# Kernel tuning notes

Hardware: AMD Instinct MI355X
Metric: run time of the kernel (lower is better)

Reference implementation:

```python
import jax, jax.numpy as jnp
import numpy as np

N, D, DOUT = 10000, 128, 128
KS, KN, KC, NCENTER, HID = 32, 16, 16, 3, 32  # HID = D // 4


def setup_inputs() -> dict:
    key = jax.random.key(0)
    ks = jax.random.split(key, 32)
    p = lambda i, shape: jax.random.normal(ks[i], shape, dtype=jnp.float32) * 0.05
    return {
        "ids": jnp.arange(N, dtype=jnp.int64) if jax.config.jax_enable_x64 else jnp.arange(N, dtype=jnp.int32),
        "feats": jax.random.normal(ks[0], (N, D), dtype=jnp.float32),
        "cluster_idx": jax.random.randint(ks[1], (N, NCENTER, KC), 0, N),
        "struct_idx": jax.random.randint(ks[2], (N, KS), 0, N),
        "epo": 100,
        # VertexConv (cluster): Transform convKK grouped conv -> (k,k,D) weight, (k,k) bias; convK1 -> (k,) weight, scalar bias
        "wKK_c": p(3, (KC, KC, D)), "bKK_c": p(4, (KC, KC)), "wK1_c": p(5, (KC,)), "bK1_c": p(6, ()),
        # VertexConv (knn)
        "wKK_n": p(7, (KN, KN, D)), "bKK_n": p(8, (KN, KN)), "wK1_n": p(9, (KN,)), "bK1_n": p(10, ()),
        # VertexConv (structure)
        "wKK_s": p(11, (KS, KS, D)), "bKK_s": p(12, (KS, KS)), "wK1_s": p(13, (KS,)), "bK1_s": p(14, ()),
        # EdgeConv attention MLP: Linear(D, D//4) -> ReLU -> Linear(D//4, 1)
        "ec_w1": p(15, (D, HID)), "ec_b1": p(16, (HID,)), "ec_w2": p(17, (HID,)), "ec_b2": p(18, ()),
        # Final Linear(D, DOUT)
        "fc_w": p(19, (D, DOUT)), "fc_b": p(20, (DOUT,)),
    }


def vertex_conv(x, wKK, bKK, wK1, bK1):
    # x: (N, k, d). Grouped Conv1d(k, k*k, d, groups=k): mult[n,i,j] = <wKK[i,j], x[n,i]> + bKK[i,j]
    mult = jnp.einsum("nid,ijd->nij", x, wKK) + bKK
    mult = jax.nn.softmax(mult, axis=-1)                 # softmax over last dim
    transformed = jnp.einsum("nij,njd->nid", mult, x)    # (N, k, d)
    # Conv1d(k, 1, 1): weighted sum over the k channels
    return jnp.einsum("nkd,k->nd", transformed, wK1) + bK1


def reference(ids, feats, cluster_idx, struct_idx, epo,
              wKK_c, bKK_c, wK1_c, bK1_c,
              wKK_n, bKK_n, wK1_n, bK1_n,
              wKK_s, bKK_s, wK1_s, bK1_s,
              ec_w1, ec_b1, ec_w2, ec_b2, fc_w, fc_b):
    # epo=100 >= all warmups -> all three hyperedge branches active (static).
    # --- cluster hyperedges (precomputed kmeans index table) ---
    c_feats = feats[cluster_idx[ids]]                    # (N, n_center, kc, d)
    hyperedge = [vertex_conv(c_feats[:, c], wKK_c, bKK_c, wK1_c, bK1_c)
                 for c in range(NCENTER)]
    # --- knn hyperedge: cosine similarity + topk (cos_dis) ---
    nrm = jnp.maximum(jnp.linalg.norm(feats, axis=1, keepdims=True), 1e-12)
    xn = feats / nrm
    sim = xn @ xn.T                                      # (N, N) -- memory-dominant
    _, knn_idx = jax.lax.top_k(sim, KN)                  # (N, kn)
    hyperedge.append(vertex_conv(feats[knn_idx[ids]], wKK_n, bKK_n, wK1_n, bK1_n))
    # --- structure hyperedge (precomputed sampled edge_dict table) ---
    hyperedge.append(vertex_conv(feats[struct_idx[ids]], wKK_s, bKK_s, wK1_s, bK1_s))
    x = jnp.stack(hyperedge, axis=1)                     # (N, t, d), t = n_center + 2
    # EdgeConv: MLP attention over the t hyperedges, softmax along t, weighted sum
    h = jax.nn.relu(jnp.einsum("ntd,dh->nth", x, ec_w1) + ec_b1)
    scores = jax.nn.softmax(jnp.einsum("nth,h->nt", h, ec_w2) + ec_b2, axis=1)
    agg = jnp.einsum("nt,ntd->nd", scores, x)            # (N, d)
    # final fc + relu (dropout = identity in eval)
    return jax.nn.relu(agg @ fc_w + fc_b)
```

## Files before the change

kernel.cpp:

```cpp
#include <hip/hip_runtime.h>
#include <cmath>


#define N_NODES 10000
#define D 128
#define DQ 32
#define NCB 3
#define T_HE 5
#define HID_SZ 32
#define NCH 16
#define CHUNK 625
#define TILE 64
#define TPC 10
#define TOPK 16
#define TOPM 32

typedef __attribute__((ext_vector_type(8))) short short8;
typedef __attribute__((ext_vector_type(8))) _Float16 half8;
typedef __attribute__((ext_vector_type(4))) float f32x4;
typedef __attribute__((ext_vector_type(16))) float f32x16;

__device__ __forceinline__ unsigned bf16rne(float f) {
  unsigned u = __float_as_uint(f);
  return (u + 0x7FFFu + ((u >> 16) & 1u)) >> 16;
}

__global__ __launch_bounds__(256) void kpre(const float* __restrict__ feats,
                                            const float* __restrict__ wc,
                                            const float* __restrict__ wn,
                                            const float* __restrict__ wstr,
                                            unsigned short* __restrict__ xnh,
                                            _Float16* __restrict__ fH16,
                                            double* __restrict__ normD,
                                            _Float16* __restrict__ wH16) {
  int bx = blockIdx.x;
  int tid = threadIdx.x;
  if (bx < 2500) {
    int n = bx * 4 + (tid >> 6);
    int lane = tid & 63;
    float2 v = ((const float2*)(feats + (size_t)n * D))[lane];
    _Float16 p2[2] = {(_Float16)v.x, (_Float16)v.y};
    ((unsigned*)(fH16 + (size_t)n * D))[lane] = *(const unsigned*)p2;
    double ss = (double)v.x * (double)v.x + (double)v.y * (double)v.y;
#pragma unroll
    for (int o = 32; o > 0; o >>= 1) ss += __shfl_xor(ss, o);
    double nd = fmax(sqrt(ss), 1e-12);
    if (lane == 0) normD[n] = nd;
    float inv = (float)(1.0 / nd);
    ((unsigned*)(xnh + (size_t)n * D))[lane] = bf16rne(v.x * inv) | (bf16rne(v.y * inv) << 16);
  } else {
    int p = (bx - 2500) * 256 + tid;
    if (p >= 98304) return;
    int e = p * 2;
    float2 v;
    if (e < 32768) v = *(const float2*)(wc + e);
    else if (e < 65536) v = *(const float2*)(wn + (e - 32768));
    else v = *(const float2*)(wstr + (e - 65536));
    _Float16 p2[2] = {(_Float16)v.x, (_Float16)v.y};
    ((unsigned*)wH16)[p] = *(const unsigned*)p2;
  }
}

__device__ __forceinline__ void ceu(unsigned& a, unsigned& b) {
  unsigned lo = min(a, b), hi = max(a, b);
  a = lo; b = hi;
}
__device__ __forceinline__ void ceu64(unsigned long long& a, unsigned long long& b) {
  unsigned long long lo = min(a, b), hi = max(a, b);
  a = lo; b = hi;
}
__device__ __forceinline__ void oems16_asc(unsigned (&v)[16]) {
  ceu(v[0], v[1]); ceu(v[2], v[3]); ceu(v[0], v[2]); ceu(v[1], v[3]); ceu(v[1], v[2]);
  ceu(v[4], v[5]); ceu(v[6], v[7]); ceu(v[4], v[6]); ceu(v[5], v[7]); ceu(v[5], v[6]);
  ceu(v[0], v[4]); ceu(v[2], v[6]); ceu(v[2], v[4]); ceu(v[1], v[5]); ceu(v[3], v[7]);
  ceu(v[3], v[5]); ceu(v[1], v[2]); ceu(v[3], v[4]); ceu(v[5], v[6]);
  ceu(v[8], v[9]); ceu(v[10], v[11]); ceu(v[8], v[10]); ceu(v[9], v[11]); ceu(v[9], v[10]);
  ceu(v[12], v[13]); ceu(v[14], v[15]); ceu(v[12], v[14]); ceu(v[13], v[15]); ceu(v[13], v[14]);
  ceu(v[8], v[12]); ceu(v[10], v[14]); ceu(v[10], v[12]); ceu(v[9], v[13]); ceu(v[11], v[15]);
  ceu(v[11], v[13]); ceu(v[9], v[10]); ceu(v[11], v[12]); ceu(v[13], v[14]);
  ceu(v[0], v[8]); ceu(v[4], v[12]); ceu(v[4], v[8]); ceu(v[2], v[10]); ceu(v[6], v[14]);
  ceu(v[6], v[10]); ceu(v[2], v[4]); ceu(v[6], v[8]); ceu(v[10], v[12]);
  ceu(v[1], v[9]); ceu(v[5], v[13]); ceu(v[5], v[9]); ceu(v[3], v[11]); ceu(v[7], v[15]);
  ceu(v[7], v[11]); ceu(v[3], v[5]); ceu(v[7], v[9]); ceu(v[11], v[13]);
  ceu(v[1], v[2]); ceu(v[3], v[4]); ceu(v[5], v[6]); ceu(v[7], v[8]); ceu(v[9], v[10]);
  ceu(v[11], v[12]); ceu(v[13], v[14]);
}
__device__ __forceinline__ void merge16_asc(unsigned (&run)[16], const unsigned (&b)[16]) {
  unsigned m[16];
#pragma unroll
  for (int i = 0; i < 16; i++) m[i] = max(run[i], b[15 - i]);
#pragma unroll
  for (int j = 8; j > 0; j >>= 1) {
#pragma unroll
    for (int i = 0; i < 16; i++) {
      if ((i & j) == 0) ceu(m[i], m[i + j]);
    }
  }
#pragma unroll
  for (int i = 0; i < 16; i++) run[i] = m[i];
}

__device__ __forceinline__ void vc16_body(int tid, int n0, int tslot,
    int* idxLm, float* coefPm, float* coefSm,
    const _Float16* __restrict__ fH16, const _Float16* __restrict__ wH16,
    const int* __restrict__ idxTab, int istr, int ioff, int woff,
    const float* __restrict__ bKK, const float* __restrict__ wK1,
    const float* __restrict__ bK1p, float* __restrict__ hx) {
  int w = tid >> 6, lane = tid & 63, l15 = lane & 15, quad = lane >> 4;
  const half8* fH = (const half8*)fH16;
  {
    int nn = tid >> 4, i = tid & 15;
    idxLm[nn * 33 + i] = idxTab[(size_t)(n0 + nn) * istr + ioff + i];
  }
  __syncthreads();
  const half8* wHv = (const half8*)(wH16 + woff);
  f32x4 coef = {0.f, 0.f, 0.f, 0.f};
#pragma unroll
  for (int ii = 0; ii < 4; ii++) {
    int i = w * 4 + ii;
    int rowi = idxLm[l15 * 33 + i];
    float bkk = bKK[i * 16 + l15];
    f32x4 acc = {0.f, 0.f, 0.f, 0.f};
#pragma unroll
    for (int kc = 0; kc < 4; kc++) {
      half8 ah = fH[(size_t)rowi * 16 + kc * 4 + quad];
      half8 bh = wHv[((size_t)i * 16 + l15) * 16 + kc * 4 + quad];
      acc = __builtin_amdgcn_mfma_f32_16x16x32_f16(ah, bh, acc, 0, 0, 0);
    }
    float wki = wK1[i];
#pragma unroll
    for (int r = 0; r < 4; r++) {
      float v = acc[r] + bkk;
      float mx = v;
#pragma unroll
      for (int msk = 1; msk < 16; msk <<= 1) mx = fmaxf(mx, __shfl_xor(mx, msk));
      float e = __expf(v - mx);
      float s = e;
#pragma unroll
      for (int msk = 1; msk < 16; msk <<= 1) s += __shfl_xor(s, msk);
      coef[r] += wki * (e / s);
    }
  }
#pragma unroll
  for (int r = 0; r < 4; r++) coefPm[(w * 16 + quad * 4 + r) * 33 + l15] = coef[r];
  __syncthreads();
  {
    int nn = tid >> 4, j = tid & 15;
    coefSm[nn * 33 + j] = coefPm[(nn) * 33 + j] + coefPm[(16 + nn) * 33 + j] +
                          coefPm[(32 + nn) * 33 + j] + coefPm[(48 + nn) * 33 + j];
  }
  __syncthreads();
  {
    int nl = tid >> 4, g = tid & 15;
    float bk1 = bK1p[0];
    float a8[8];
#pragma unroll
    for (int t = 0; t < 8; t++) a8[t] = bk1;
    for (int j = 0; j < 16; j++) {
      float cf = coefSm[nl * 33 + j];
      int rowj = idxLm[nl * 33 + j];
      half8 xv = fH[(size_t)rowj * 16 + g];
#pragma unroll
      for (int e = 0; e < 8; e++) a8[e] = fmaf(cf, (float)xv[e], a8[e]);
    }
    int node = n0 + nl;
    float4* o = (float4*)(hx + ((size_t)node * T_HE + tslot) * D + g * 8);
    o[0] = make_float4(a8[0], a8[1], a8[2], a8[3]);
    o[1] = make_float4(a8[4], a8[5], a8[6], a8[7]);
  }
}

__device__ __forceinline__ void vc32_body(int tid, int n0,
    int* idxLm, float* coefPm, float* coefSm,
    const _Float16* __restrict__ fH16, const _Float16* __restrict__ wH16,
    const int* __restrict__ struct_idx,
    const float* __restrict__ bKK_s, const float* __restrict__ wK1_s,
    const float* __restrict__ bK1_s, float* __restrict__ hx) {
  int w = tid >> 6, lane = tid & 63, l15 = lane & 15, quad = lane >> 4;
  const half8* fH = (const half8*)fH16;
  for (int e = tid; e < 512; e += 256) {
    int nn = e >> 5, i = e & 31;
    idxLm[nn * 33 + i] = struct_idx[(size_t)(n0 + nn) * 32 + i];
  }
  __syncthreads();
  const half8* wHv = (const half8*)(wH16 + 65536);
  f32x4 coef0 = {0.f, 0.f, 0.f, 0.f};
  f32x4 coef1 = {0.f, 0.f, 0.f, 0.f};
#pragma unroll
  for (int ii = 0; ii < 8; ii++) {
    int i = w * 8 + ii;
    int rowi = idxLm[l15 * 33 + i];
    float bk0 = bKK_s[i * 32 + l15];
    float bk1v = bKK_s[i * 32 + 16 + l15];
    f32x4 a0 = {0.f, 0.f, 0.f, 0.f};
    f32x4 a1 = {0.f, 0.f, 0.f, 0.f};
#pragma unroll
    for (int kc = 0; kc < 4; kc++) {
      half8 ah = fH[(size_t)rowi * 16 + kc * 4 + quad];
      half8 b0 = wHv[((size_t)i * 32 + l15) * 16 + kc * 4 + quad];
      half8 b1 = wHv[((size_t)i * 32 + 16 + l15) * 16 + kc * 4 + quad];
      a0 = __builtin_amdgcn_mfma_f32_16x16x32_f16(ah, b0, a0, 0, 0, 0);
      a1 = __builtin_amdgcn_mfma_f32_16x16x32_f16(ah, b1, a1, 0, 0, 0);
    }
    float wki = wK1_s[i];
#pragma unroll
    for (int r = 0; r < 4; r++) {
      float v0 = a0[r] + bk0, v1 = a1[r] + bk1v;
      float mx = fmaxf(v0, v1);
#pragma unroll
      for (int msk = 1; msk < 16; msk <<= 1) mx = fmaxf(mx, __shfl_xor(mx, msk));
      float e0 = __expf(v0 - mx), e1 = __expf(v1 - mx);
      float s = e0 + e1;
#pragma unroll
      for (int msk = 1; msk < 16; msk <<= 1) s += __shfl_xor(s, msk);
      float inv = wki / s;
      coef0[r] += e0 * inv;
      coef1[r] += e1 * inv;
    }
  }
#pragma unroll
  for (int r = 0; r < 4; r++) {
    coefPm[(w * 16 + quad * 4 + r) * 33 + l15] = coef0[r];
    coefPm[(w * 16 + quad * 4 + r) * 33 + l15 + 16] = coef1[r];
  }
  __syncthreads();
  for (int e = tid; e < 512; e += 256) {
    int nn = e >> 5, j = e & 31;
    coefSm[nn * 33 + j] = coefPm[nn * 33 + j] + coefPm[(16 + nn) * 33 + j] +
                          coefPm[(32 + nn) * 33 + j] + coefPm[(48 + nn) * 33 + j];
  }
  __syncthreads();
  {
    int nl = tid >> 4, g = tid & 15;
    float bk1 = bK1_s[0];
    float a8[8];
#pragma unroll
    for (int t = 0; t < 8; t++) a8[t] = bk1;
    for (int j = 0; j < 32; j++) {
      float cf = coefSm[nl * 33 + j];
      int rowj = idxLm[nl * 33 + j];
      half8 xv = fH[(size_t)rowj * 16 + g];
#pragma unroll
      for (int e = 0; e < 8; e++) a8[e] = fmaf(cf, (float)xv[e], a8[e]);
    }
    int node = n0 + nl;
    float4* o = (float4*)(hx + ((size_t)node * T_HE + 4) * D + g * 8);
    o[0] = make_float4(a8[0], a8[1], a8[2], a8[3]);
    o[1] = make_float4(a8[4], a8[5], a8[6], a8[7]);
  }
}

__global__ __launch_bounds__(256, 3) void ksimvc(
    const unsigned short* __restrict__ xnh, unsigned* __restrict__ cand,
    const _Float16* __restrict__ fH16, const _Float16* __restrict__ wH16,
    const int* __restrict__ cluster_idx, const int* __restrict__ struct_idx,
    const float* __restrict__ bKK_c, const float* __restrict__ bKK_s,
    const float* __restrict__ wK1_c, const float* __restrict__ bK1_c,
    const float* __restrict__ wK1_s, const float* __restrict__ bK1_s,
    float* __restrict__ hx) {
  __shared__ __align__(16) unsigned char smem[16384];
  int bx = blockIdx.x;
  int tid = threadIdx.x;
  int r3 = bx % 3, q3 = bx / 3;
  if (r3 == 0) {
    int sid = q3;
    int rb = sid % 79, chunk = sid / 79;
    int w = tid >> 6, lane = tid & 63, l31 = lane & 31, lh = lane >> 5;
    int row0 = rb * 128 + w * 32;
    int cbase = chunk * CHUNK;
    int ci = tid >> 2, q = tid & 3;
    short8* bp = (short8*)smem;
    const short8* bv = (const short8*)smem;

    short8 afr[8];
    {
      int ar = min(row0 + l31, N_NODES - 1);
      const short8* ap = (const short8*)(xnh + (size_t)ar * D);
#pragma unroll
      for (int ks = 0; ks < 8; ks++) afr[ks] = ap[ks * 2 + lh];
    }

    unsigned run[16];
#pragma unroll
    for (int s = 0; s < 16; s++) run[s] = 0u;

    short8 G[4];
    {
      int gcol = min(cbase + ci, N_NODES - 1);
      const short8* gp = (const short8*)(xnh + (size_t)gcol * D);
#pragma unroll
      for (int i = 0; i < 4; i++) G[i] = gp[q * 4 + i];
    }

#pragma unroll 1
    for (int ti = 0; ti < TPC; ti++) {
      __syncthreads();
      {
#pragma unroll
        for (int i = 0; i < 4; i++) bp[(q * 4 + i) * 64 + ci] = G[i];
      }
      if (ti + 1 < TPC) {
        int gcol = min(cbase + (ti + 1) * TILE + ci, N_NODES - 1);
        const short8* gp = (const short8*)(xnh + (size_t)gcol * D);
#pragma unroll
        for (int i = 0; i < 4; i++) G[i] = gp[q * 4 + i];
      }
      __syncthreads();

#pragma unroll
      for (int ni = 0; ni < 2; ni++) {
        f32x16 acc;
#pragma unroll
        for (int r = 0; r < 16; r++) acc[r] = 2.0f;
#pragma unroll
        for (int ks = 0; ks < 8; ks++) {
          short8 af = bv[(ks * 2 + lh) * 64 + ni * 32 + l31];
          acc = __builtin_amdgcn_mfma_f32_32x32x16_bf16(af, afr[ks], acc, 0, 0, 0);
        }
        unsigned bt[16];
#pragma unroll
        for (int reg = 0; reg < 16; reg++) {
          int m = (reg & 3) + 8 * (reg >> 2) + 4 * lh;
          unsigned bb = __float_as_uint(acc[reg]);
          bt[reg] = (bb & 0xFFFFFC00u) | (unsigned)(ti * TILE + ni * 32 + m);
        }
        if (ti == TPC - 1) {
#pragma unroll
          for (int reg = 0; reg < 16; reg++) {
            int m = (reg & 3) + 8 * (reg >> 2) + 4 * lh;
            if (ni * 32 + m >= CHUNK - (TPC - 1) * TILE) bt[reg] = 0u;
          }
        }
        oems16_asc(bt);
        merge16_asc(run, bt);
      }
    }
    {
      unsigned other[16];
#pragma unroll
      for (int s = 0; s < 16; s++) other[s] = (unsigned)__shfl_xor((int)run[s], 32);
      merge16_asc(run, other);
    }
    int grow = row0 + l31;
    if (lh == 0 && grow < N_NODES) {
      unsigned* o = cand + ((size_t)chunk * N_NODES + grow) * 16;
#pragma unroll
      for (int i = 0; i < 16; i += 4)
        *(uint4*)(o + i) = make_uint4(run[i], run[i + 1], run[i + 2], run[i + 3]);
    }
  } else {
    int vid = q3 * 2 + (r3 - 1);
    if (vid >= 2500) return;
    int zz = vid / 625, bi = vid - zz * 625;
    int n0 = bi * 16;
    int* idxLm = (int*)smem;
    float* coefPm = (float*)(smem + 2112);
    float* coefSm = (float*)(smem + 10560);
    if (zz < 3) {
      vc16_body(tid, n0, zz, idxLm, coefPm, coefSm, fH16, wH16,
                cluster_idx, NCB * 16, zz * 16, 0, bKK_c, wK1_c, bK1_c, hx);
    } else {
      vc32_body(tid, n0, idxLm, coefPm, coefSm, fH16, wH16,
                struct_idx, bKK_s, wK1_s, bK1_s, hx);
    }
  }
}

__global__ __launch_bounds__(256, 4) void kvc3(
    const _Float16* __restrict__ fH16, const _Float16* __restrict__ wH16,
    const int* __restrict__ knn,
    const float* __restrict__ bKK_n, const float* __restrict__ wK1_n,
    const float* __restrict__ bK1_n, float* __restrict__ hx) {
  __shared__ __align__(16) unsigned char smem[12672];
  int* idxLm = (int*)smem;
  float* coefPm = (float*)(smem + 2112);
  float* coefSm = (float*)(smem + 10560);
  vc16_body(threadIdx.x, blockIdx.x * 16, 3, idxLm, coefPm, coefSm, fH16, wH16,
            knn, 16, 0, 32768, bKK_n, wK1_n, bK1_n, hx);
}

__global__ __launch_bounds__(256) void kmerge(const unsigned* __restrict__ cand,
                                              int* __restrict__ candIdx) {
  int t4 = blockIdx.x * 256 + threadIdx.x;
  int row = t4 >> 2, sub = t4 & 3;
  if (row >= N_NODES) return;
  unsigned long long run[TOPM];
#pragma unroll
  for (int s = 0; s < TOPM; s++) run[s] = 0ull;
  const uint4* c4 = (const uint4*)cand;
#pragma unroll
  for (int t = 0; t < 4; t++) {
    int ch = sub * 4 + t;
    unsigned b[16];
#pragma unroll
    for (int q = 0; q < 4; q++) {
      uint4 v = c4[((size_t)ch * N_NODES + row) * 4 + q];
      b[q * 4 + 0] = v.x; b[q * 4 + 1] = v.y;
      b[q * 4 + 2] = v.z; b[q * 4 + 3] = v.w;
    }
    unsigned base = (unsigned)(ch * CHUNK);
    unsigned long long b64[16];
#pragma unroll
    for (int s = 0; s < 16; s++) {
      unsigned k = b[s];
      b64[s] = ((unsigned long long)(k >> 10) << 32) |
               (unsigned long long)(base + (k & 1023u));
    }
#pragma unroll
    for (int i = 0; i < 16; i++) run[i] = max(run[i], b64[15 - i]);
#pragma unroll
    for (int j = 16; j > 0; j >>= 1)
#pragma unroll
      for (int i = 0; i < TOPM; i++)
        if ((i & j) == 0) ceu64(run[i], run[i + j]);
  }
#pragma unroll
  for (int off = 1; off <= 2; off <<= 1) {
    unsigned long long oth[TOPM];
#pragma unroll
    for (int s = 0; s < TOPM; s++) {
      unsigned lo = (unsigned)(run[s] & 0xFFFFFFFFull);
      unsigned hi = (unsigned)(run[s] >> 32);
      lo = (unsigned)__shfl_xor((int)lo, off);
      hi = (unsigned)__shfl_xor((int)hi, off);
      oth[s] = ((unsigned long long)hi << 32) | (unsigned long long)lo;
    }
#pragma unroll
    for (int i = 0; i < TOPM; i++) run[i] = max(run[i], oth[TOPM - 1 - i]);
#pragma unroll
    for (int j = 16; j > 0; j >>= 1)
#pragma unroll
      for (int i = 0; i < TOPM; i++)
        if ((i & j) == 0) ceu64(run[i], run[i + j]);
  }
  if (sub == 0) {
    int4* o4 = (int4*)(candIdx + (size_t)row * TOPM);
#pragma unroll
    for (int s = 0; s < TOPM; s += 4) {
      int4 o;
      o.x = (int)(unsigned)(run[s + 0] & 0xFFFFFFFFull);
      o.y = (int)(unsigned)(run[s + 1] & 0xFFFFFFFFull);
      o.z = (int)(unsigned)(run[s + 2] & 0xFFFFFFFFull);
      o.w = (int)(unsigned)(run[s + 3] & 0xFFFFFFFFull);
      o4[s >> 2] = o;
    }
  }
}

__global__ __launch_bounds__(256) void krerank(const float* __restrict__ feats,
                                               const double* __restrict__ normD,
                                               const int* __restrict__ candIdx,
                                               int* __restrict__ knn) {
  __shared__ float rowF[D];
  __shared__ double simL[TOPM];
  __shared__ int idxL[TOPM];
  int row = blockIdx.x;
  int tid = threadIdx.x;
  if (tid < DQ)
    ((float4*)rowF)[tid] = ((const float4*)(feats + (size_t)row * D))[tid];
  int c = tid >> 3, part = tid & 7;
  int cnd = candIdx[(size_t)row * TOPM + c];
  __syncthreads();
  const float4* f4 = (const float4*)(feats + (size_t)cnd * D);
  double acc = 0.0;
#pragma unroll
  for (int g = 0; g < 4; g++) {
    float4 v = f4[part * 4 + g];
    const float* rf = &rowF[(part * 4 + g) * 4];
    acc = fma((double)v.x, (double)rf[0], acc);
    acc = fma((double)v.y, (double)rf[1], acc);
    acc = fma((double)v.z, (double)rf[2], acc);
    acc = fma((double)v.w, (double)rf[3], acc);
  }
  acc += __shfl_down(acc, 4);
  acc += __shfl_down(acc, 2);
  acc += __shfl_down(acc, 1);
  if (part == 0) {
    simL[c] = acc / (normD[row] * normD[cnd]);
    idxL[c] = cnd;
  }
  __syncthreads();
  if (tid < TOPM) {
    double s = simL[tid];
    int idx = idxL[tid];
    int rank = 0;
#pragma unroll
    for (int o = 0; o < TOPM; o++) {
      double so = simL[o];
      int io = idxL[o];
      rank += (so > s || (so == s && io < idx)) ? 1 : 0;
    }
    if (rank < TOPK) knn[(size_t)row * TOPK + rank] = idx;
  }
}

__global__ __launch_bounds__(256) void kfinal(const float* __restrict__ hx,
    const float* __restrict__ w1, const float* __restrict__ b1,
    const float* __restrict__ w2, const float* __restrict__ b2p,
    const float* __restrict__ fcw, const float* __restrict__ fcb,
    float* __restrict__ out) {
  __shared__ float xL[8][T_HE][D];
  __shared__ float hL[8][T_HE][HID_SZ];
  __shared__ float scL[8][T_HE];
  __shared__ float aggL[8][D];
  int tid = threadIdx.x;
  int n0 = blockIdx.x * 8;
  const float4* hx4 = (const float4*)hx;
  for (int q = tid; q < 8 * T_HE * DQ; q += 256) {
    int nn = q / (T_HE * DQ);
    int rem = q - nn * (T_HE * DQ);
    int t = rem / DQ;
    int dq = rem & 31;
    int node = n0 + nn;
    float4 val = make_float4(0.f, 0.f, 0.f, 0.f);
    if (node < N_NODES) val = hx4[((size_t)node * T_HE + t) * DQ + dq];
    *(float4*)&xL[nn][t][dq << 2] = val;
  }
  __syncthreads();
  for (int q = tid; q < 8 * T_HE * HID_SZ; q += 256) {
    int nn = q / (T_HE * HID_SZ);
    int rem = q - nn * (T_HE * HID_SZ);
    int t = rem / HID_SZ;
    int hh = rem & (HID_SZ - 1);
    float acc = b1[hh];
    const float4* xv4 = (const float4*)xL[nn][t];
    for (int dq = 0; dq < 32; dq++) {
      float4 xv = xv4[dq];
      int db = dq * 4;
      acc = fmaf(xv.x, w1[(db + 0) * HID_SZ + hh], acc);
      acc = fmaf(xv.y, w1[(db + 1) * HID_SZ + hh], acc);
      acc = fmaf(xv.z, w1[(db + 2) * HID_SZ + hh], acc);
      acc = fmaf(xv.w, w1[(db + 3) * HID_SZ + hh], acc);
    }
    hL[nn][t][hh] = fmaxf(acc, 0.f);
  }
  __syncthreads();
  if (tid < 8 * T_HE) {
    int nn = tid / T_HE, t = tid % T_HE;
    float acc = b2p[0];
    for (int hh = 0; hh < HID_SZ; hh++) acc = fmaf(hL[nn][t][hh], w2[hh], acc);
    scL[nn][t] = acc;
  }
  __syncthreads();
  if (tid < 8) {
    float mx = -1e30f;
#pragma unroll
    for (int t = 0; t < T_HE; t++) mx = fmaxf(mx, scL[tid][t]);
    float e[T_HE];
    float s = 0.f;
#pragma unroll
    for (int t = 0; t < T_HE; t++) { e[t] = expf(scL[tid][t] - mx); s += e[t]; }
    float inv = 1.f / s;
#pragma unroll
    for (int t = 0; t < T_HE; t++) scL[tid][t] = e[t] * inv;
  }
  __syncthreads();
  {
    int nn = tid >> 5, dq = tid & 31;
    float4 acc = make_float4(0.f, 0.f, 0.f, 0.f);
#pragma unroll
    for (int t = 0; t < T_HE; t++) {
      float sw = scL[nn][t];
      float4 xv = *(const float4*)&xL[nn][t][dq << 2];
      acc.x = fmaf(sw, xv.x, acc.x);
      acc.y = fmaf(sw, xv.y, acc.y);
      acc.z = fmaf(sw, xv.z, acc.z);
      acc.w = fmaf(sw, xv.w, acc.w);
    }
    *(float4*)&aggL[nn][dq << 2] = acc;
  }
  __syncthreads();
  {
    int dout = tid & 127, g = tid >> 7;
    float a0 = fcb[dout], a1 = a0, a2 = a0, a3 = a0;
    for (int dq = 0; dq < 32; dq++) {
      int db = dq * 4;
      float wv0 = fcw[(db + 0) * 128 + dout];
      float wv1 = fcw[(db + 1) * 128 + dout];
      float wv2 = fcw[(db + 2) * 128 + dout];
      float wv3 = fcw[(db + 3) * 128 + dout];
      float4 v0 = *(const float4*)&aggL[g * 4 + 0][db];
      float4 v1 = *(const float4*)&aggL[g * 4 + 1][db];
      float4 v2 = *(const float4*)&aggL[g * 4 + 2][db];
      float4 v3 = *(const float4*)&aggL[g * 4 + 3][db];
      a0 = fmaf(v0.x, wv0, fmaf(v0.y, wv1, fmaf(v0.z, wv2, fmaf(v0.w, wv3, a0))));
      a1 = fmaf(v1.x, wv0, fmaf(v1.y, wv1, fmaf(v1.z, wv2, fmaf(v1.w, wv3, a1))));
      a2 = fmaf(v2.x, wv0, fmaf(v2.y, wv1, fmaf(v2.z, wv2, fmaf(v2.w, wv3, a2))));
      a3 = fmaf(v3.x, wv0, fmaf(v3.y, wv1, fmaf(v3.z, wv2, fmaf(v3.w, wv3, a3))));
    }
    int nb = n0 + g * 4;
    if (nb + 0 < N_NODES) out[(size_t)(nb + 0) * 128 + dout] = fmaxf(a0, 0.f);
    if (nb + 1 < N_NODES) out[(size_t)(nb + 1) * 128 + dout] = fmaxf(a1, 0.f);
    if (nb + 2 < N_NODES) out[(size_t)(nb + 2) * 128 + dout] = fmaxf(a2, 0.f);
    if (nb + 3 < N_NODES) out[(size_t)(nb + 3) * 128 + dout] = fmaxf(a3, 0.f);
  }
}

extern "C" void kernel_launch(void* const* d_in, const int* in_sizes, int n_in,
                              void* d_out, int out_size, void* d_ws, size_t ws_size,
                              hipStream_t stream) {
  (void)in_sizes; (void)n_in; (void)out_size; (void)ws_size;
  const float* feats       = (const float*)d_in[1];
  const int*   cluster_idx = (const int*)d_in[2];
  const int*   struct_idx  = (const int*)d_in[3];
  const float* wKK_c = (const float*)d_in[5];
  const float* bKK_c = (const float*)d_in[6];
  const float* wK1_c = (const float*)d_in[7];
  const float* bK1_c = (const float*)d_in[8];
  const float* wKK_n = (const float*)d_in[9];
  const float* bKK_n = (const float*)d_in[10];
  const float* wK1_n = (const float*)d_in[11];
  const float* bK1_n = (const float*)d_in[12];
  const float* wKK_s = (const float*)d_in[13];
  const float* bKK_s = (const float*)d_in[14];
  const float* wK1_s = (const float*)d_in[15];
  const float* bK1_s = (const float*)d_in[16];
  const float* ec_w1 = (const float*)d_in[17];
  const float* ec_b1 = (const float*)d_in[18];
  const float* ec_w2 = (const float*)d_in[19];
  const float* ec_b2 = (const float*)d_in[20];
  const float* fc_w  = (const float*)d_in[21];
  const float* fc_b  = (const float*)d_in[22];
  float* out = (float*)d_out;

  char* wsb = (char*)d_ws;
  unsigned short* xnh = (unsigned short*)(wsb);
  _Float16* fH16 = (_Float16*)(wsb + 2560000);
  _Float16* wH16 = (_Float16*)(wsb + 5120000);
  double* normD = (double*)(wsb + 5513216);
  unsigned* cand = (unsigned*)(wsb + 5593216);
  int* candIdx = (int*)(wsb + 15833216);
  int* knnIdx = (int*)(wsb + 17113216);
  float* hx = (float*)(wsb + 17753216);

  kpre<<<2884, 256, 0, stream>>>(feats, wKK_c, wKK_n, wKK_s,
                                 xnh, fH16, normD, wH16);
  ksimvc<<<3792, 256, 0, stream>>>(xnh, cand, fH16, wH16, cluster_idx, struct_idx,
                                   bKK_c, bKK_s, wK1_c, bK1_c, wK1_s, bK1_s, hx);
  kmerge<<<(N_NODES * 4 + 255) / 256, 256, 0, stream>>>(cand, candIdx);
  krerank<<<N_NODES, 256, 0, stream>>>(feats, normD, candIdx, knnIdx);
  kvc3<<<625, 256, 0, stream>>>(fH16, wH16, knnIdx, bKK_n, wK1_n, bK1_n, hx);
  kfinal<<<1250, 256, 0, stream>>>(hx, ec_w1, ec_b1, ec_w2, ec_b2, fc_w, fc_b, out);
}
```

Measured before the change: 333.2 us.

## Fuse candidate merge, fp64 rerank and knn vertex conv into one kernel

Replaces the separate kmerge, krerank and kvc3 launches with one kernel, kmrv, that handles 16 rows per block. The first wave merges candidate lists while the other waves stage row features in shared memory. The block then reranks in fp64, writes the top-16 indices straight into shared memory and runs the vertex conv core. This removes two launches and the global round trips for candIdx and knnIdx. In exchange the merge stage runs on only one wave per block, and the grid shrinks to 625 blocks, so there is less parallelism for the rerank.

Measured after the change: 359.2 us. 1.08x slower.

```diff
diff --git a/kernel.cpp b/kernel.cpp
--- a/kernel.cpp
+++ b/kernel.cpp
@@ -100,74 +100,83 @@
   for (int i = 0; i < 16; i++) run[i] = m[i];
 }
 
+__device__ __forceinline__ void vc16_core(int tid, int n0, int tslot,
+    int* idxLm, float* coefPm, float* coefSm,
+    const _Float16* __restrict__ fH16, const _Float16* __restrict__ wH16,
+    int woff, const float* __restrict__ bKK, const float* __restrict__ wK1,
+    const float* __restrict__ bK1p, float* __restrict__ hx) {
+  int w = tid >> 6, lane = tid & 63, l15 = lane & 15, quad = lane >> 4;
+  const half8* fH = (const half8*)fH16;
+  const half8* wHv = (const half8*)(wH16 + woff);
+  f32x4 coef = {0.f, 0.f, 0.f, 0.f};
+#pragma unroll
+  for (int ii = 0; ii < 4; ii++) {
+    int i = w * 4 + ii;
+    int rowi = idxLm[l15 * 33 + i];
+    float bkk = bKK[i * 16 + l15];
+    f32x4 acc = {0.f, 0.f, 0.f, 0.f};
+#pragma unroll
+    for (int kc = 0; kc < 4; kc++) {
+      half8 ah = fH[(size_t)rowi * 16 + kc * 4 + quad];
+      half8 bh = wHv[((size_t)i * 16 + l15) * 16 + kc * 4 + quad];
+      acc = __builtin_amdgcn_mfma_f32_16x16x32_f16(ah, bh, acc, 0, 0, 0);
+    }
+    float wki = wK1[i];
+#pragma unroll
+    for (int r = 0; r < 4; r++) {
+      float v = acc[r] + bkk;
+      float mx = v;
+#pragma unroll
+      for (int msk = 1; msk < 16; msk <<= 1) mx = fmaxf(mx, __shfl_xor(mx, msk));
+      float e = __expf(v - mx);
+      float s = e;
+#pragma unroll
+      for (int msk = 1; msk < 16; msk <<= 1) s += __shfl_xor(s, msk);
+      coef[r] += wki * (e / s);
+    }
+  }
+#pragma unroll
+  for (int r = 0; r < 4; r++) coefPm[(w * 16 + quad * 4 + r) * 33 + l15] = coef[r];
+  __syncthreads();
+  {
+    int nn = tid >> 4, j = tid & 15;
+    coefSm[nn * 33 + j] = coefPm[(nn) * 33 + j] + coefPm[(16 + nn) * 33 + j] +
+                          coefPm[(32 + nn) * 33 + j] + coefPm[(48 + nn) * 33 + j];
+  }
+  __syncthreads();
+  {
+    int nl = tid >> 4, g = tid & 15;
+    float bk1 = bK1p[0];
+    float a8[8];
+#pragma unroll
+    for (int t = 0; t < 8; t++) a8[t] = bk1;
+    for (int j = 0; j < 16; j++) {
+      float cf = coefSm[nl * 33 + j];
+      int rowj = idxLm[nl * 33 + j];
+      half8 xv = fH[(size_t)rowj * 16 + g];
+#pragma unroll
+      for (int e = 0; e < 8; e++) a8[e] = fmaf(cf, (float)xv[e], a8[e]);
+    }
+    int node = n0 + nl;
+    float4* o = (float4*)(hx + ((size_t)node * T_HE + tslot) * D + g * 8);
+    o[0] = make_float4(a8[0], a8[1], a8[2], a8[3]);
+    o[1] = make_float4(a8[4], a8[5], a8[6], a8[7]);
+  }
+}
+
 __device__ __forceinline__ void vc16_body(int tid, int n0, int tslot,
     int* idxLm, float* coefPm, float* coefSm,
     const _Float16* __restrict__ fH16, const _Float16* __restrict__ wH16,
     const int* __restrict__ idxTab, int istr, int ioff, int woff,
     const float* __restrict__ bKK, const float* __restrict__ wK1,
     const float* __restrict__ bK1p, float* __restrict__ hx) {
-  int w = tid >> 6, lane = tid & 63, l15 = lane & 15, quad = lane >> 4;
-  const half8* fH = (const half8*)fH16;
   {
     int nn = tid >> 4, i = tid & 15;
     idxLm[nn * 33 + i] = idxTab[(size_t)(n0 + nn) * istr + ioff + i];
   }
   __syncthreads();
-  const half8* wHv = (const half8*)(wH16 + woff);
-  f32x4 coef = {0.f, 0.f, 0.f, 0.f};
-#pragma unroll
-  for (int ii = 0; ii < 4; ii++) {
-    int i = w * 4 + ii;
-    int rowi = idxLm[l15 * 33 + i];
-    float bkk = bKK[i * 16 + l15];
-    f32x4 acc = {0.f, 0.f, 0.f, 0.f};
-#pragma unroll
-    for (int kc = 0; kc < 4; kc++) {
-      half8 ah = fH[(size_t)rowi * 16 + kc * 4 + quad];
-      half8 bh = wHv[((size_t)i * 16 + l15) * 16 + kc * 4 + quad];
-      acc = __builtin_amdgcn_mfma_f32_16x16x32_f16(ah, bh, acc, 0, 0, 0);
-    }
-    float wki = wK1[i];
-#pragma unroll
-    for (int r = 0; r < 4; r++) {
-      float v = acc[r] + bkk;
-      float mx = v;
-#pragma unroll
-      for (int msk = 1; msk < 16; msk <<= 1) mx = fmaxf(mx, __shfl_xor(mx, msk));
-      float e = __expf(v - mx);
-      float s = e;
-#pragma unroll
-      for (int msk = 1; msk < 16; msk <<= 1) s += __shfl_xor(s, msk);
-      coef[r] += wki * (e / s);
-    }
-  }
-#pragma unroll
-  for (int r = 0; r < 4; r++) coefPm[(w * 16 + quad * 4 + r) * 33 + l15] = coef[r];
-  __syncthreads();
-  {
-    int nn = tid >> 4, j = tid & 15;
-    coefSm[nn * 33 + j] = coefPm[(nn) * 33 + j] + coefPm[(16 + nn) * 33 + j] +
-                          coefPm[(32 + nn) * 33 + j] + coefPm[(48 + nn) * 33 + j];
-  }
-  __syncthreads();
-  {
-    int nl = tid >> 4, g = tid & 15;
-    float bk1 = bK1p[0];
-    float a8[8];
-#pragma unroll
-    for (int t = 0; t < 8; t++) a8[t] = bk1;
-    for (int j = 0; j < 16; j++) {
-      float cf = coefSm[nl * 33 + j];
-      int rowj = idxLm[nl * 33 + j];
-      half8 xv = fH[(size_t)rowj * 16 + g];
-#pragma unroll
-      for (int e = 0; e < 8; e++) a8[e] = fmaf(cf, (float)xv[e], a8[e]);
-    }
-    int node = n0 + nl;
-    float4* o = (float4*)(hx + ((size_t)node * T_HE + tslot) * D + g * 8);
-    o[0] = make_float4(a8[0], a8[1], a8[2], a8[3]);
-    o[1] = make_float4(a8[4], a8[5], a8[6], a8[7]);
-  }
+  vc16_core(tid, n0, tslot, idxLm, coefPm, coefSm, fH16, wH16, woff,
+            bKK, wK1, bK1p, hx);
 }
 
 __device__ __forceinline__ void vc32_body(int tid, int n0,
@@ -366,132 +375,133 @@
   }
 }
 
-__global__ __launch_bounds__(256, 4) void kvc3(
+__global__ __launch_bounds__(256) void kmrv(
+    const unsigned* __restrict__ cand,
+    const float* __restrict__ feats,
+    const double* __restrict__ normD,
     const _Float16* __restrict__ fH16, const _Float16* __restrict__ wH16,
-    const int* __restrict__ knn,
     const float* __restrict__ bKK_n, const float* __restrict__ wK1_n,
     const float* __restrict__ bK1_n, float* __restrict__ hx) {
-  __shared__ __align__(16) unsigned char smem[12672];
+  __shared__ __align__(16) unsigned char smem[18816];
   int* idxLm = (int*)smem;
   float* coefPm = (float*)(smem + 2112);
   float* coefSm = (float*)(smem + 10560);
-  vc16_body(threadIdx.x, blockIdx.x * 16, 3, idxLm, coefPm, coefSm, fH16, wH16,
-            knn, 16, 0, 32768, bKK_n, wK1_n, bK1_n, hx);
-}
-
-__global__ __launch_bounds__(256) void kmerge(const unsigned* __restrict__ cand,
-                                              int* __restrict__ candIdx) {
-  int t4 = blockIdx.x * 256 + threadIdx.x;
-  int row = t4 >> 2, sub = t4 & 3;
-  if (row >= N_NODES) return;
-  unsigned long long run[TOPM];
-#pragma unroll
-  for (int s = 0; s < TOPM; s++) run[s] = 0ull;
-  const uint4* c4 = (const uint4*)cand;
-#pragma unroll
-  for (int t = 0; t < 4; t++) {
-    int ch = sub * 4 + t;
-    unsigned b[16];
-#pragma unroll
-    for (int q = 0; q < 4; q++) {
-      uint4 v = c4[((size_t)ch * N_NODES + row) * 4 + q];
-      b[q * 4 + 0] = v.x; b[q * 4 + 1] = v.y;
-      b[q * 4 + 2] = v.z; b[q * 4 + 3] = v.w;
-    }
-    unsigned base = (unsigned)(ch * CHUNK);
-    unsigned long long b64[16];
-#pragma unroll
-    for (int s = 0; s < 16; s++) {
-      unsigned k = b[s];
-      b64[s] = ((unsigned long long)(k >> 10) << 32) |
-               (unsigned long long)(base + (k & 1023u));
-    }
-#pragma unroll
-    for (int i = 0; i < 16; i++) run[i] = max(run[i], b64[15 - i]);
-#pragma unroll
-    for (int j = 16; j > 0; j >>= 1)
-#pragma unroll
-      for (int i = 0; i < TOPM; i++)
-        if ((i & j) == 0) ceu64(run[i], run[i + j]);
-  }
-#pragma unroll
-  for (int off = 1; off <= 2; off <<= 1) {
-    unsigned long long oth[TOPM];
-#pragma unroll
-    for (int s = 0; s < TOPM; s++) {
-      unsigned lo = (unsigned)(run[s] & 0xFFFFFFFFull);
-      unsigned hi = (unsigned)(run[s] >> 32);
-      lo = (unsigned)__shfl_xor((int)lo, off);
-      hi = (unsigned)__shfl_xor((int)hi, off);
-      oth[s] = ((unsigned long long)hi << 32) | (unsigned long long)lo;
-    }
-#pragma unroll
-    for (int i = 0; i < TOPM; i++) run[i] = max(run[i], oth[TOPM - 1 - i]);
-#pragma unroll
-    for (int j = 16; j > 0; j >>= 1)
-#pragma unroll
-      for (int i = 0; i < TOPM; i++)
-        if ((i & j) == 0) ceu64(run[i], run[i + j]);
-  }
-  if (sub == 0) {
-    int4* o4 = (int4*)(candIdx + (size_t)row * TOPM);
-#pragma unroll
-    for (int s = 0; s < TOPM; s += 4) {
-      int4 o;
-      o.x = (int)(unsigned)(run[s + 0] & 0xFFFFFFFFull);
-      o.y = (int)(unsigned)(run[s + 1] & 0xFFFFFFFFull);
-      o.z = (int)(unsigned)(run[s + 2] & 0xFFFFFFFFull);
-      o.w = (int)(unsigned)(run[s + 3] & 0xFFFFFFFFull);
-      o4[s >> 2] = o;
-    }
-  }
-}
-
-__global__ __launch_bounds__(256) void krerank(const float* __restrict__ feats,
-                                               const double* __restrict__ normD,
-                                               const int* __restrict__ candIdx,
-                                               int* __restrict__ knn) {
-  __shared__ float rowF[D];
-  __shared__ double simL[TOPM];
-  __shared__ int idxL[TOPM];
-  int row = blockIdx.x;
+  float* rowF = (float*)(smem + 2112);
+  double* simL = (double*)(smem + 12672);
+  int* cidxL = (int*)(smem + 16768);
   int tid = threadIdx.x;
-  if (tid < DQ)
-    ((float4*)rowF)[tid] = ((const float4*)(feats + (size_t)row * D))[tid];
-  int c = tid >> 3, part = tid & 7;
-  int cnd = candIdx[(size_t)row * TOPM + c];
-  __syncthreads();
-  const float4* f4 = (const float4*)(feats + (size_t)cnd * D);
-  double acc = 0.0;
-#pragma unroll
-  for (int g = 0; g < 4; g++) {
-    float4 v = f4[part * 4 + g];
-    const float* rf = &rowF[(part * 4 + g) * 4];
-    acc = fma((double)v.x, (double)rf[0], acc);
-    acc = fma((double)v.y, (double)rf[1], acc);
-    acc = fma((double)v.z, (double)rf[2], acc);
-    acc = fma((double)v.w, (double)rf[3], acc);
-  }
-  acc += __shfl_down(acc, 4);
-  acc += __shfl_down(acc, 2);
-  acc += __shfl_down(acc, 1);
-  if (part == 0) {
-    simL[c] = acc / (normD[row] * normD[cnd]);
-    idxL[c] = cnd;
-  }
-  __syncthreads();
-  if (tid < TOPM) {
-    double s = simL[tid];
-    int idx = idxL[tid];
+  int n0 = blockIdx.x * 16;
+
+  if (tid < 64) {
+    int row16 = tid >> 2, sub = tid & 3;
+    int row = n0 + row16;
+    unsigned long long run[TOPM];
+#pragma unroll
+    for (int s = 0; s < TOPM; s++) run[s] = 0ull;
+    const uint4* c4 = (const uint4*)cand;
+#pragma unroll
+    for (int t = 0; t < 4; t++) {
+      int ch = sub * 4 + t;
+      unsigned b[16];
+#pragma unroll
+      for (int q = 0; q < 4; q++) {
+        uint4 v = c4[((size_t)ch * N_NODES + row) * 4 + q];
+        b[q * 4 + 0] = v.x; b[q * 4 + 1] = v.y;
+        b[q * 4 + 2] = v.z; b[q * 4 + 3] = v.w;
+      }
+      unsigned base = (unsigned)(ch * CHUNK);
+      unsigned long long b64[16];
+#pragma unroll
+      for (int s = 0; s < 16; s++) {
+        unsigned k = b[s];
+        b64[s] = ((unsigned long long)(k >> 10) << 32) |
+                 (unsigned long long)(base + (k & 1023u));
+      }
+#pragma unroll
+      for (int i = 0; i < 16; i++) run[i] = max(run[i], b64[15 - i]);
+#pragma unroll
+      for (int j = 16; j > 0; j >>= 1)
+#pragma unroll
+        for (int i = 0; i < TOPM; i++)
+          if ((i & j) == 0) ceu64(run[i], run[i + j]);
+    }
+#pragma unroll
+    for (int off = 1; off <= 2; off <<= 1) {
+      unsigned long long oth[TOPM];
+#pragma unroll
+      for (int s = 0; s < TOPM; s++) {
+        unsigned lo = (unsigned)(run[s] & 0xFFFFFFFFull);
+        unsigned hi = (unsigned)(run[s] >> 32);
+        lo = (unsigned)__shfl_xor((int)lo, off);
+        hi = (unsigned)__shfl_xor((int)hi, off);
+        oth[s] = ((unsigned long long)hi << 32) | (unsigned long long)lo;
+      }
+#pragma unroll
+      for (int i = 0; i < TOPM; i++) run[i] = max(run[i], oth[TOPM - 1 - i]);
+#pragma unroll
+      for (int j = 16; j > 0; j >>= 1)
+#pragma unroll
+        for (int i = 0; i < TOPM; i++)
+          if ((i & j) == 0) ceu64(run[i], run[i + j]);
+    }
+    if (sub == 0) {
+#pragma unroll
+      for (int s = 0; s < TOPM; s++)
+        cidxL[row16 * TOPM + s] = (int)(unsigned)(run[s] & 0xFFFFFFFFull);
+    }
+  } else {
+    const float4* f4 = (const float4*)feats;
+    float4* r4 = (float4*)rowF;
+    for (int v = tid - 64; v < 512; v += 192) {
+      int r16 = v >> 5, dq = v & 31;
+      r4[r16 * 32 + dq] = f4[((size_t)(n0 + r16)) * 32 + dq];
+    }
+  }
+  __syncthreads();
+
+  {
+    int pc = tid >> 2;
+    int part = tid & 3;
+#pragma unroll 1
+    for (int pass = 0; pass < 8; pass++) {
+      int r16 = pass * 2 + (pc >> 5);
+      int c = pc & 31;
+      int cnd = cidxL[r16 * TOPM + c];
+      const float4* f4 = (const float4*)(feats + (size_t)cnd * D) + part * 8;
+      const float4* rf4 = (const float4*)(rowF + r16 * D) + part * 8;
+      double acc = 0.0;
+#pragma unroll
+      for (int g = 0; g < 8; g++) {
+        float4 v = f4[g], r = rf4[g];
+        acc = fma((double)v.x, (double)r.x, acc);
+        acc = fma((double)v.y, (double)r.y, acc);
+        acc = fma((double)v.z, (double)r.z, acc);
+        acc = fma((double)v.w, (double)r.w, acc);
+      }
+      acc += __shfl_xor(acc, 1);
+      acc += __shfl_xor(acc, 2);
+      if (part == 0)
+        simL[r16 * TOPM + c] = acc / (normD[n0 + r16] * normD[cnd]);
+    }
+  }
+  __syncthreads();
+  for (int t = tid; t < 512; t += 256) {
+    int r16 = t >> 5, c = t & 31;
+    double s = simL[r16 * TOPM + c];
+    int idx = cidxL[r16 * TOPM + c];
     int rank = 0;
 #pragma unroll
     for (int o = 0; o < TOPM; o++) {
-      double so = simL[o];
-      int io = idxL[o];
+      double so = simL[r16 * TOPM + o];
+      int io = cidxL[r16 * TOPM + o];
       rank += (so > s || (so == s && io < idx)) ? 1 : 0;
     }
-    if (rank < TOPK) knn[(size_t)row * TOPK + rank] = idx;
-  }
+    if (rank < TOPK) idxLm[r16 * 33 + rank] = idx;
+  }
+  __syncthreads();
+
+  vc16_core(tid, n0, 3, idxLm, coefPm, coefSm, fH16, wH16, 32768,
+            bKK_n, wK1_n, bK1_n, hx);
 }
 
 __global__ __launch_bounds__(256) void kfinal(const float* __restrict__ hx,
@@ -629,16 +639,13 @@
   _Float16* wH16 = (_Float16*)(wsb + 5120000);
   double* normD = (double*)(wsb + 5513216);
   unsigned* cand = (unsigned*)(wsb + 5593216);
-  int* candIdx = (int*)(wsb + 15833216);
-  int* knnIdx = (int*)(wsb + 17113216);
   float* hx = (float*)(wsb + 17753216);
 
   kpre<<<2884, 256, 0, stream>>>(feats, wKK_c, wKK_n, wKK_s,
                                  xnh, fH16, normD, wH16);
   ksimvc<<<3792, 256, 0, stream>>>(xnh, cand, fH16, wH16, cluster_idx, struct_idx,
                                    bKK_c, bKK_s, wK1_c, bK1_c, wK1_s, bK1_s, hx);
-  kmerge<<<(N_NODES * 4 + 255) / 256, 256, 0, stream>>>(cand, candIdx);
-  krerank<<<N_NODES, 256, 0, stream>>>(feats, normD, candIdx, knnIdx);
-  kvc3<<<625, 256, 0, stream>>>(fH16, wH16, knnIdx, bKK_n, wK1_n, bK1_n, hx);
+  kmrv<<<625, 256, 0, stream>>>(cand, feats, normD, fH16, wH16,
+                                bKK_n, wK1_n, bK1_n, hx);
   kfinal<<<1250, 256, 0, stream>>>(hx, ec_w1, ec_b1, ec_w2, ec_b2, fc_w, fc_b, out);
 }
```
